# Kernel optimization log

Measured on AMD Instinct MI355X. Metric: run time of the kernel, lower is better.

## Reference

```python
import jax, jax.numpy as jnp
import numpy as np


def setup_inputs() -> dict:
    key = jax.random.key(0)
    k1, k2, k3 = jax.random.split(key, 3)
    B, S_enc, S_dec, D = 8, 4096, 4096, 128
    b = jax.random.normal(k1, (B, S_enc, D), dtype=jnp.float32)
    h = jax.random.normal(k2, (B, S_dec, D), dtype=jnp.float32)
    W_b = jax.random.normal(k3, (D, D), dtype=jnp.float32) * (1.0 / np.sqrt(D))
    return {"b": b, "h": h, "W_b": W_b}


def reference(b, h, W_b):
    # tmp1 = h @ W_b : [B, S_dec, D]
    tmp1 = jnp.einsum('btd,de->bte', h, W_b)
    # scores = tmp1 @ b^T : [B, S_dec, S_enc]
    scores = jnp.einsum('bte,bse->bts', tmp1, b)
    attn = jax.nn.softmax(scores, axis=-1)
    # weighted sum over encoder positions (the original does this via a huge
    # tile/broadcast/multiply/reduce_sum; math is a batched matmul)
    cxt = jnp.einsum('bts,bsd->btd', attn, b)
    return cxt
```

## Files before the change

kernel.cpp:

```cpp
#include <hip/hip_runtime.h>

typedef _Float16 half2v __attribute__((ext_vector_type(2)));
typedef _Float16 half4 __attribute__((ext_vector_type(4)));
typedef _Float16 half8 __attribute__((ext_vector_type(8)));
typedef float floatx4 __attribute__((ext_vector_type(4)));

#define B_   8
#define SE   4096
#define SD   4096
#define D_   128
#define NT   64
#define LDB  136
#define LOG2E 1.44269504f

__device__ __forceinline__ void cp16_async(const _Float16* g, _Float16* l) {
    __builtin_amdgcn_global_load_lds((const __attribute__((address_space(1))) unsigned int*)g,
                                     (__attribute__((address_space(3))) unsigned int*)l, 16, 0, 0);
}

__device__ __forceinline__ float dot2acc(half2v a, half2v b, float c) {
#if __has_builtin(__builtin_amdgcn_fdot2)
    return __builtin_amdgcn_fdot2(a, b, c, false);
#else
    return c + (float)a[0] * (float)b[0] + (float)a[1] * (float)b[1];
#endif
}

__global__ __launch_bounds__(256) void wprep(const float* __restrict__ W,
                                             _Float16* __restrict__ Wt16,
                                             _Float16* __restrict__ Wtlo) {
    int i = blockIdx.x * 256 + threadIdx.x;
    int d = i >> 7, e = i & 127;
    float w = W[i];
    _Float16 hi = (_Float16)w;
    Wt16[e * 128 + d] = hi;
    Wtlo[e * 128 + d] = (_Float16)(w - (float)hi);
}

__global__ __launch_bounds__(256) void bprep(const float* __restrict__ b,
                                             _Float16* __restrict__ kc,
                                             _Float16* __restrict__ vT) {
    __shared__ _Float16 bs[64 * LDB];
    const int bb = blockIdx.y, s0 = blockIdx.x * 64;
    const int tid = threadIdx.x;

    const float* bg = b + ((size_t)bb * SE + s0) * D_;
    _Float16* kg = kc + ((size_t)bb * SE + s0) * D_;
    #pragma unroll
    for (int it = 0; it < 4; ++it) {
        int idx = tid + it * 256;
        int row = idx >> 4, seg = idx & 15;
        const float* src = bg + row * D_ + seg * 8;
        float4 a = *(const float4*)src;
        float4 c = *(const float4*)(src + 4);
        half8 hv;
        hv[0] = (_Float16)a.x; hv[1] = (_Float16)a.y; hv[2] = (_Float16)a.z; hv[3] = (_Float16)a.w;
        hv[4] = (_Float16)c.x; hv[5] = (_Float16)c.y; hv[6] = (_Float16)c.z; hv[7] = (_Float16)c.w;
        *(half8*)(kg + row * D_ + seg * 8) = hv;
        *(half8*)(bs + row * LDB + seg * 8) = hv;
    }
    __syncthreads();

    const int sg = tid & 7, dg = tid >> 3;
    half4 rowv[8];
    #pragma unroll
    for (int j = 0; j < 8; ++j)
        rowv[j] = *(const half4*)(bs + (sg * 8 + j) * LDB + dg * 4);
    #pragma unroll
    for (int dd = 0; dd < 4; ++dd) {
        half8 o;
        #pragma unroll
        for (int j = 0; j < 8; ++j) o[j] = rowv[j][dd];
        *(half8*)(vT + ((size_t)bb * D_ + dg * 4 + dd) * SE + s0 + sg * 8) = o;
    }
}

__global__ __launch_bounds__(256, 2) void flash(const float* __restrict__ h,
                                                const _Float16* __restrict__ Wt16,
                                                const _Float16* __restrict__ Wtlo,
                                                const _Float16* __restrict__ kc,
                                                const _Float16* __restrict__ vT,
                                                float* __restrict__ out) {
    __shared__ _Float16 KV[2][16384];

    const int bb   = blockIdx.y;
    const int q0   = blockIdx.x * 64;
    const int tid  = threadIdx.x;
    const int wave = tid >> 6;
    const int wq   = wave >> 1;
    const int ws   = wave & 1;
    const int lane = tid & 63;
    const int l15  = lane & 15;
    const int quad = lane >> 4;

    const _Float16* kbase = kc + (size_t)bb * SE * D_;
    const _Float16* vbase = vT + (size_t)bb * D_ * SE;

    int koff[4], voff[4];
    #pragma unroll
    for (int it = 0; it < 4; ++it) {
        int i = it * 256 + wave * 64 + lane;
        int kr = i >> 4, kpp = i & 15;
        int km = kr & 15;
        int srow = (kr & 32) + ((km >> 2) << 3) + (((kr >> 4) & 1) << 2) + (km & 3);
        koff[it] = srow * D_ + ((kpp ^ km) * 8);
        int vr = i >> 3, vpp = i & 7;
        voff[it] = vr * SE + ((vpp ^ (vr & 7)) * 8);
    }

    const _Float16* kA0[4]; const _Float16* kA1[4];
    const _Float16 *vB0, *vB1;
    #pragma unroll
    for (int ks = 0; ks < 4; ++ks) {
        int o = l15 * 128 + (((ks * 4 + quad) ^ l15) * 8) + ws * 4096;
        kA0[ks] = &KV[0][o]; kA1[ks] = &KV[1][o];
    }
    {
        int o = 8192 + l15 * 64 + (((ws * 4 + quad) ^ (l15 & 7)) * 8);
        vB0 = &KV[0][o]; vB1 = &KV[1][o];
    }

    {
        _Float16* buf0 = &KV[0][0];
        #pragma unroll
        for (int it = 0; it < 4; ++it) {
            cp16_async(kbase + koff[it], buf0 + (it * 256 + wave * 64) * 8);
            cp16_async(vbase + voff[it], buf0 + 8192 + (it * 256 + wave * 64) * 8);
        }
    }

    _Float16* hs = &KV[1][0];
    {
        const float* hg = h + ((size_t)bb * SD + q0) * D_;
        #pragma unroll
        for (int it = 0; it < 4; ++it) {
            int idx = tid + it * 256;
            int row = idx >> 4, seg = idx & 15;
            const float* src = hg + row * D_ + seg * 8;
            float4 a = *(const float4*)src;
            float4 c = *(const float4*)(src + 4);
            half8 hv;
            hv[0] = (_Float16)a.x; hv[1] = (_Float16)a.y; hv[2] = (_Float16)a.z; hv[3] = (_Float16)a.w;
            hv[4] = (_Float16)c.x; hv[5] = (_Float16)c.y; hv[6] = (_Float16)c.z; hv[7] = (_Float16)c.w;
            *(half8*)(hs + row * LDB + seg * 8) = hv;
        }
    }
    __syncthreads();
    half8 qf0[4], qf1[4];
    {
        half8 af[4];
        #pragma unroll
        for (int ks = 0; ks < 4; ++ks)
            af[ks] = *(const half8*)(hs + (wave * 16 + l15) * LDB + ks * 32 + quad * 8);
        floatx4 acc[8];
        #pragma unroll
        for (int nt = 0; nt < 8; ++nt) acc[nt] = (floatx4){0.f, 0.f, 0.f, 0.f};
        #pragma unroll
        for (int ks = 0; ks < 4; ++ks) {
            #pragma unroll
            for (int nt = 0; nt < 8; ++nt) {
                half8 bh = *(const half8*)(Wt16 + (size_t)(nt * 16 + l15) * 128 + ks * 32 + quad * 8);
                half8 bl = *(const half8*)(Wtlo + (size_t)(nt * 16 + l15) * 128 + ks * 32 + quad * 8);
                acc[nt] = __builtin_amdgcn_mfma_f32_16x16x32_f16(af[ks], bh, acc[nt], 0, 0, 0);
                acc[nt] = __builtin_amdgcn_mfma_f32_16x16x32_f16(af[ks], bl, acc[nt], 0, 0, 0);
            }
        }
        __syncthreads();
        #pragma unroll
        for (int nt = 0; nt < 8; ++nt)
            #pragma unroll
            for (int r = 0; r < 4; ++r)
                hs[(wave * 16 + quad * 4 + r) * LDB + nt * 16 + l15] =
                    (_Float16)(acc[nt][r] * LOG2E);
        __syncthreads();
        #pragma unroll
        for (int ks = 0; ks < 4; ++ks) {
            qf0[ks] = *(const half8*)(hs + (wq * 32 + l15) * LDB + ks * 32 + quad * 8);
            qf1[ks] = *(const half8*)(hs + (wq * 32 + 16 + l15) * LDB + ks * 32 + quad * 8);
        }
    }

    floatx4 acc_o0[8], acc_o1[8];
    #pragma unroll
    for (int dt = 0; dt < 8; ++dt) {
        acc_o0[dt] = (floatx4){0.f, 0.f, 0.f, 0.f};
        acc_o1[dt] = (floatx4){0.f, 0.f, 0.f, 0.f};
    }
    float nm0 = 0.f, nm1 = 0.f;
    float lp0 = 0.f, lp1 = 0.f;
    const half2v one2 = { (_Float16)1.f, (_Float16)1.f };

#define RESCALE(MV, NM, LP, ACCS, ACCO)                                               \
    { float mr = fmaxf((MV), __shfl_xor((MV), 16, 64));                               \
      mr = fmaxf(mr, __shfl_xor(mr, 32, 64));                                         \
      float delta = fmaxf(mr, 0.f);                                                   \
      float alpha = exp2f(-delta);                                                    \
      LP *= alpha;                                                                    \
      float ab[4];                                                                    \
      _Pragma("unroll")                                                               \
      for (int r = 0; r < 4; ++r) ab[r] = __shfl(alpha, quad * 4 + r, 64);            \
      _Pragma("unroll")                                                               \
      for (int dt = 0; dt < 8; ++dt)                                                  \
        _Pragma("unroll")                                                             \
        for (int r = 0; r < 4; ++r) ACCO[dt][r] *= ab[r];                             \
      _Pragma("unroll")                                                               \
      for (int stl = 0; stl < 2; ++stl)                                               \
        _Pragma("unroll")                                                             \
        for (int r = 0; r < 4; ++r) ACCS[stl][r] -= delta;                            \
      NM -= delta; }

#define SOFTPACK(ACCS, LP, PA)                                                        \
    { float p0 = exp2f(ACCS[0][0]), p1 = exp2f(ACCS[0][1]);                           \
      float p2 = exp2f(ACCS[0][2]), p3 = exp2f(ACCS[0][3]);                           \
      float p4 = exp2f(ACCS[1][0]), p5 = exp2f(ACCS[1][1]);                           \
      float p6 = exp2f(ACCS[1][2]), p7 = exp2f(ACCS[1][3]);                           \
      half2v c0 = __builtin_bit_cast(half2v, __builtin_amdgcn_cvt_pkrtz(p0, p1));     \
      half2v c1 = __builtin_bit_cast(half2v, __builtin_amdgcn_cvt_pkrtz(p2, p3));     \
      half2v c2 = __builtin_bit_cast(half2v, __builtin_amdgcn_cvt_pkrtz(p4, p5));     \
      half2v c3 = __builtin_bit_cast(half2v, __builtin_amdgcn_cvt_pkrtz(p6, p7));     \
      LP = dot2acc(c0, one2, LP);                                                     \
      LP = dot2acc(c1, one2, LP);                                                     \
      LP = dot2acc(c2, one2, LP);                                                     \
      LP = dot2acc(c3, one2, LP);                                                     \
      PA[0] = c0[0]; PA[1] = c0[1]; PA[2] = c1[0]; PA[3] = c1[1];                     \
      PA[4] = c2[0]; PA[5] = c2[1]; PA[6] = c3[0]; PA[7] = c3[1]; }

#define STEP(T, KA, VBP, NBUF)                                                        \
  {                                                                                   \
    __syncthreads();                  \
    if ((T) + 1 < SE / NT) {                                                          \
      const _Float16* kt = kbase + (size_t)((T) + 1) * (NT * D_);                     \
      const _Float16* vt = vbase + (size_t)((T) + 1) * NT;                            \
      _Float16* bufn = (NBUF);                                                        \
      _Pragma("unroll")                                                               \
      for (int it = 0; it < 4; ++it) {                                                \
        cp16_async(kt + koff[it], bufn + (it * 256 + wave * 64) * 8);                 \
        cp16_async(vt + voff[it], bufn + 8192 + (it * 256 + wave * 64) * 8);          \
      }                                                                               \
    }                                                                                 \
    floatx4 accs0[2], accs1[2];                                                       \
    accs0[0] = (floatx4){nm0, nm0, nm0, nm0}; accs0[1] = accs0[0];                    \
    accs1[0] = (floatx4){nm1, nm1, nm1, nm1}; accs1[1] = accs1[0];                    \
    _Pragma("unroll")                                                                 \
    for (int ks = 0; ks < 4; ++ks) {                                                  \
      half8 af0 = *(const half8*)(KA[ks]);                                            \
      half8 af1 = *(const half8*)(KA[ks] + 2048);                                     \
      accs0[0] = __builtin_amdgcn_mfma_f32_16x16x32_f16(af0, qf0[ks], accs0[0], 0, 0, 0); \
      accs0[1] = __builtin_amdgcn_mfma_f32_16x16x32_f16(af1, qf0[ks], accs0[1], 0, 0, 0); \
      accs1[0] = __builtin_amdgcn_mfma_f32_16x16x32_f16(af0, qf1[ks], accs1[0], 0, 0, 0); \
      accs1[1] = __builtin_amdgcn_mfma_f32_16x16x32_f16(af1, qf1[ks], accs1[1], 0, 0, 0); \
    }                                                                                 \
    float mv0 = fmaxf(fmaxf(fmaxf(accs0[0][0], accs0[0][1]), fmaxf(accs0[0][2], accs0[0][3])), \
                      fmaxf(fmaxf(accs0[1][0], accs0[1][1]), fmaxf(accs0[1][2], accs0[1][3]))); \
    float mv1 = fmaxf(fmaxf(fmaxf(accs1[0][0], accs1[0][1]), fmaxf(accs1[0][2], accs1[0][3])), \
                      fmaxf(fmaxf(accs1[1][0], accs1[1][1]), fmaxf(accs1[1][2], accs1[1][3]))); \
    if (__ballot((mv0 > 11.5f) || (mv1 > 11.5f)) != 0ull) {                           \
      RESCALE(mv0, nm0, lp0, accs0, acc_o0);                                          \
      RESCALE(mv1, nm1, lp1, accs1, acc_o1);                                          \
    }                                                                                 \
    half8 pA0, pA1;                                                                   \
    SOFTPACK(accs0, lp0, pA0);                                                        \
    SOFTPACK(accs1, lp1, pA1);                                                        \
    _Pragma("unroll")                                                                 \
    for (int dt = 0; dt < 8; ++dt) {                                                  \
      half8 vf = *(const half8*)((VBP) + dt * 1024);                                  \
      acc_o0[dt] = __builtin_amdgcn_mfma_f32_16x16x32_f16(pA0, vf, acc_o0[dt], 0, 0, 0); \
      acc_o1[dt] = __builtin_amdgcn_mfma_f32_16x16x32_f16(pA1, vf, acc_o1[dt], 0, 0, 0); \
    }                                                                                 \
  }

    for (int t = 0; t < SE / NT; t += 2) {
        STEP(t,     kA0, vB0, &KV[1][0]);
        STEP(t + 1, kA1, vB1, &KV[0][0]);
    }
#undef STEP

    const float m_q0 = -nm0, m_q1 = -nm1;
    float lo0, lo1;
    {
        float l = lp0;
        l += __shfl_xor(l, 16, 64);
        l += __shfl_xor(l, 32, 64);
        lo0 = l;
        l = lp1;
        l += __shfl_xor(l, 16, 64);
        l += __shfl_xor(l, 32, 64);
        lo1 = l;
    }

    __syncthreads();
    float* Ob = (float*)&KV[0][0];
    float* ml = (float*)&KV[1][0];

    if (ws == 1) {
        #pragma unroll
        for (int dt = 0; dt < 8; ++dt) {
            *(floatx4*)(Ob + (((wq * 2 + 0) * 8 + dt) * 64 + lane) * 4) = acc_o0[dt];
            *(floatx4*)(Ob + (((wq * 2 + 1) * 8 + dt) * 64 + lane) * 4) = acc_o1[dt];
        }
        if (quad == 0) {
            *(float2*)(ml + (wq * 32 + l15) * 2)      = make_float2(m_q0, lo0);
            *(float2*)(ml + (wq * 32 + 16 + l15) * 2) = make_float2(m_q1, lo1);
        }
    }
    __syncthreads();
    if (ws == 0) {
#define MERGE(ACC, MQ, LO, QQ)                                                        \
      { float m0r[4], l0r[4], m1r[4], l1r[4];                                         \
        _Pragma("unroll")                                                             \
        for (int r = 0; r < 4; ++r) {                                                 \
            m0r[r] = __shfl((MQ), quad * 4 + r, 64);                                  \
            l0r[r] = __shfl((LO), quad * 4 + r, 64);                                  \
            float2 p = *(float2*)(ml + (wq * 32 + (QQ) * 16 + quad * 4 + r) * 2);     \
            m1r[r] = p.x; l1r[r] = p.y;                                               \
        }                                                                             \
        float a0[4], a1[4], inv[4];                                                   \
        _Pragma("unroll")                                                             \
        for (int r = 0; r < 4; ++r) {                                                 \
            float mm = fmaxf(m0r[r], m1r[r]);                                         \
            a0[r] = exp2f(m0r[r] - mm);                                               \
            a1[r] = exp2f(m1r[r] - mm);                                               \
            inv[r] = 1.f / (l0r[r] * a0[r] + l1r[r] * a1[r]);                         \
        }                                                                             \
        float* orow = out + ((size_t)bb * SD + q0 + wq * 32 + (QQ) * 16 + quad * 4) * D_; \
        _Pragma("unroll")                                                             \
        for (int dt = 0; dt < 8; ++dt) {                                              \
            floatx4 o1 = *(floatx4*)(Ob + (((wq * 2 + (QQ)) * 8 + dt) * 64 + lane) * 4); \
            _Pragma("unroll")                                                         \
            for (int r = 0; r < 4; ++r)                                               \
                orow[(size_t)r * D_ + dt * 16 + l15] =                                \
                    (ACC[dt][r] * a0[r] + o1[r] * a1[r]) * inv[r];                    \
        } }
        MERGE(acc_o0, m_q0, lo0, 0);
        MERGE(acc_o1, m_q1, lo1, 1);
#undef MERGE
    }
#undef RESCALE
#undef SOFTPACK
}

extern "C" void kernel_launch(void* const* d_in, const int* in_sizes, int n_in,
                              void* d_out, int out_size, void* d_ws, size_t ws_size,
                              hipStream_t stream) {
    const float* b = (const float*)d_in[0];
    const float* h = (const float*)d_in[1];
    const float* W = (const float*)d_in[2];
    float* out = (float*)d_out;

    _Float16* Wt16 = (_Float16*)d_ws;
    _Float16* Wtlo = Wt16 + 128 * 128;
    _Float16* kc   = Wtlo + 128 * 128;
    _Float16* vT   = kc + (size_t)B_ * SE * D_;

    wprep<<<64, 256, 0, stream>>>(W, Wt16, Wtlo);
    bprep<<<dim3(SE / 64, B_), 256, 0, stream>>>(b, kc, vT);
    flash<<<dim3(SD / 64, B_), 256, 0, stream>>>(h, Wt16, Wtlo, kc, vT, out);
}
```

Measured before the change: 199.3 us.

## Split encoder keys across two grid slices, widen blocks, add merge kernel

Splits the key/value sequence into two halves along a new grid z dimension, so each block computes partial softmax-weighted outputs and writes unnormalized results plus max/sum stats to global scratch. A separate merge kernel then combines the two partials. Blocks grow to 512 threads covering 128 queries, and the W prep is folded into bprep to save a launch. The aim is more parallelism and occupancy per key pass, at the cost of extra global traffic for the partials and one more launch.

```diff
diff --git a/kernel.cpp b/kernel.cpp
--- a/kernel.cpp
+++ b/kernel.cpp
@@ -10,6 +10,8 @@
 #define SD   4096
 #define D_   128
 #define NT   64
+#define NZ   2
+#define TILES (SE / NZ / NT)
 #define LDB  136
 #define LOG2E 1.44269504f
 
@@ -26,23 +28,28 @@
 #endif
 }
 
-__global__ __launch_bounds__(256) void wprep(const float* __restrict__ W,
+__global__ __launch_bounds__(256) void bprep(const float* __restrict__ b,
+                                             const float* __restrict__ W,
+                                             _Float16* __restrict__ kc,
+                                             _Float16* __restrict__ vT,
                                              _Float16* __restrict__ Wt16,
                                              _Float16* __restrict__ Wtlo) {
-    int i = blockIdx.x * 256 + threadIdx.x;
-    int d = i >> 7, e = i & 127;
-    float w = W[i];
-    _Float16 hi = (_Float16)w;
-    Wt16[e * 128 + d] = hi;
-    Wtlo[e * 128 + d] = (_Float16)(w - (float)hi);
-}
-
-__global__ __launch_bounds__(256) void bprep(const float* __restrict__ b,
-                                             _Float16* __restrict__ kc,
-                                             _Float16* __restrict__ vT) {
     __shared__ _Float16 bs[64 * LDB];
     const int bb = blockIdx.y, s0 = blockIdx.x * 64;
     const int tid = threadIdx.x;
+
+    if (blockIdx.x == 0) {
+        int base = bb * 2048 + tid * 8;
+        #pragma unroll
+        for (int j = 0; j < 8; ++j) {
+            int i = base + j;
+            int d = i >> 7, e = i & 127;
+            float w = W[i];
+            _Float16 hi = (_Float16)w;
+            Wt16[e * 128 + d] = hi;
+            Wtlo[e * 128 + d] = (_Float16)(w - (float)hi);
+        }
+    }
 
     const float* bg = b + ((size_t)bb * SE + s0) * D_;
     _Float16* kg = kc + ((size_t)bb * SE + s0) * D_;
@@ -75,16 +82,20 @@
     }
 }
 
-__global__ __launch_bounds__(256, 2) void flash(const float* __restrict__ h,
+__global__ __launch_bounds__(512, 4) void flash(const float* __restrict__ h,
                                                 const _Float16* __restrict__ Wt16,
                                                 const _Float16* __restrict__ Wtlo,
                                                 const _Float16* __restrict__ kc,
                                                 const _Float16* __restrict__ vT,
-                                                float* __restrict__ out) {
+                                                float* __restrict__ out,
+                                                float* __restrict__ P1,
+                                                float2* __restrict__ mlA,
+                                                float2* __restrict__ mlB) {
     __shared__ _Float16 KV[2][16384];
 
     const int bb   = blockIdx.y;
-    const int q0   = blockIdx.x * 64;
+    const int q0   = blockIdx.x * 128;
+    const int z    = blockIdx.z;
     const int tid  = threadIdx.x;
     const int wave = tid >> 6;
     const int wq   = wave >> 1;
@@ -93,13 +104,13 @@
     const int l15  = lane & 15;
     const int quad = lane >> 4;
 
-    const _Float16* kbase = kc + (size_t)bb * SE * D_;
-    const _Float16* vbase = vT + (size_t)bb * D_ * SE;
-
-    int koff[4], voff[4];
-    #pragma unroll
-    for (int it = 0; it < 4; ++it) {
-        int i = it * 256 + wave * 64 + lane;
+    const _Float16* kbase = kc + (size_t)bb * SE * D_ + (size_t)z * (SE / NZ) * D_;
+    const _Float16* vbase = vT + (size_t)bb * D_ * SE + (size_t)z * (SE / NZ);
+
+    int koff[2], voff[2];
+    #pragma unroll
+    for (int it = 0; it < 2; ++it) {
+        int i = it * 512 + wave * 64 + lane;
         int kr = i >> 4, kpp = i & 15;
         int km = kr & 15;
         int srow = (kr & 32) + ((km >> 2) << 3) + (((kr >> 4) & 1) << 2) + (km & 3);
@@ -123,18 +134,19 @@
     {
         _Float16* buf0 = &KV[0][0];
         #pragma unroll
-        for (int it = 0; it < 4; ++it) {
-            cp16_async(kbase + koff[it], buf0 + (it * 256 + wave * 64) * 8);
-            cp16_async(vbase + voff[it], buf0 + 8192 + (it * 256 + wave * 64) * 8);
+        for (int it = 0; it < 2; ++it) {
+            cp16_async(kbase + koff[it], buf0 + (it * 512 + wave * 64) * 8);
+            cp16_async(vbase + voff[it], buf0 + 8192 + (it * 512 + wave * 64) * 8);
         }
     }
 
     _Float16* hs = &KV[1][0];
+    const float* hg = h + ((size_t)bb * SD + q0) * D_;
+    half8 af[4];
     {
-        const float* hg = h + ((size_t)bb * SD + q0) * D_;
-        #pragma unroll
-        for (int it = 0; it < 4; ++it) {
-            int idx = tid + it * 256;
+        #pragma unroll
+        for (int it = 0; it < 2; ++it) {
+            int idx = tid + it * 512;
             int row = idx >> 4, seg = idx & 15;
             const float* src = hg + row * D_ + seg * 8;
             float4 a = *(const float4*)src;
@@ -144,14 +156,35 @@
             hv[4] = (_Float16)c.x; hv[5] = (_Float16)c.y; hv[6] = (_Float16)c.z; hv[7] = (_Float16)c.w;
             *(half8*)(hs + row * LDB + seg * 8) = hv;
         }
-    }
-    __syncthreads();
+        __syncthreads();
+        if (wave < 4) {
+            #pragma unroll
+            for (int ks = 0; ks < 4; ++ks)
+                af[ks] = *(const half8*)(hs + (wave * 16 + l15) * LDB + ks * 32 + quad * 8);
+        }
+        __syncthreads();
+        #pragma unroll
+        for (int it = 0; it < 2; ++it) {
+            int idx = tid + it * 512;
+            int row = idx >> 4, seg = idx & 15;
+            const float* src = hg + (row + 64) * D_ + seg * 8;
+            float4 a = *(const float4*)src;
+            float4 c = *(const float4*)(src + 4);
+            half8 hv;
+            hv[0] = (_Float16)a.x; hv[1] = (_Float16)a.y; hv[2] = (_Float16)a.z; hv[3] = (_Float16)a.w;
+            hv[4] = (_Float16)c.x; hv[5] = (_Float16)c.y; hv[6] = (_Float16)c.z; hv[7] = (_Float16)c.w;
+            *(half8*)(hs + row * LDB + seg * 8) = hv;
+        }
+        __syncthreads();
+        if (wave >= 4) {
+            #pragma unroll
+            for (int ks = 0; ks < 4; ++ks)
+                af[ks] = *(const half8*)(hs + ((wave - 4) * 16 + l15) * LDB + ks * 32 + quad * 8);
+        }
+        __syncthreads();
+    }
     half8 qf0[4], qf1[4];
     {
-        half8 af[4];
-        #pragma unroll
-        for (int ks = 0; ks < 4; ++ks)
-            af[ks] = *(const half8*)(hs + (wave * 16 + l15) * LDB + ks * 32 + quad * 8);
         floatx4 acc[8];
         #pragma unroll
         for (int nt = 0; nt < 8; ++nt) acc[nt] = (floatx4){0.f, 0.f, 0.f, 0.f};
@@ -159,24 +192,45 @@
         for (int ks = 0; ks < 4; ++ks) {
             #pragma unroll
             for (int nt = 0; nt < 8; ++nt) {
-                half8 bh = *(const half8*)(Wt16 + (size_t)(nt * 16 + l15) * 128 + ks * 32 + quad * 8);
-                half8 bl = *(const half8*)(Wtlo + (size_t)(nt * 16 + l15) * 128 + ks * 32 + quad * 8);
+                size_t wo = (size_t)(nt * 16 + l15) * 128 + ks * 32 + quad * 8;
+                half8 bh = *(const half8*)(Wt16 + wo);
+                half8 bl = *(const half8*)(Wtlo + wo);
                 acc[nt] = __builtin_amdgcn_mfma_f32_16x16x32_f16(af[ks], bh, acc[nt], 0, 0, 0);
                 acc[nt] = __builtin_amdgcn_mfma_f32_16x16x32_f16(af[ks], bl, acc[nt], 0, 0, 0);
             }
         }
-        __syncthreads();
-        #pragma unroll
-        for (int nt = 0; nt < 8; ++nt)
-            #pragma unroll
-            for (int r = 0; r < 4; ++r)
-                hs[(wave * 16 + quad * 4 + r) * LDB + nt * 16 + l15] =
-                    (_Float16)(acc[nt][r] * LOG2E);
-        __syncthreads();
-        #pragma unroll
-        for (int ks = 0; ks < 4; ++ks) {
-            qf0[ks] = *(const half8*)(hs + (wq * 32 + l15) * LDB + ks * 32 + quad * 8);
-            qf1[ks] = *(const half8*)(hs + (wq * 32 + 16 + l15) * LDB + ks * 32 + quad * 8);
+        if (wave < 4) {
+            #pragma unroll
+            for (int nt = 0; nt < 8; ++nt)
+                #pragma unroll
+                for (int r = 0; r < 4; ++r)
+                    hs[(wave * 16 + quad * 4 + r) * LDB + nt * 16 + l15] =
+                        (_Float16)(acc[nt][r] * LOG2E);
+        }
+        __syncthreads();
+        if (wq < 2) {
+            #pragma unroll
+            for (int ks = 0; ks < 4; ++ks) {
+                qf0[ks] = *(const half8*)(hs + (wq * 32 + l15) * LDB + ks * 32 + quad * 8);
+                qf1[ks] = *(const half8*)(hs + (wq * 32 + 16 + l15) * LDB + ks * 32 + quad * 8);
+            }
+        }
+        __syncthreads();
+        if (wave >= 4) {
+            #pragma unroll
+            for (int nt = 0; nt < 8; ++nt)
+                #pragma unroll
+                for (int r = 0; r < 4; ++r)
+                    hs[((wave - 4) * 16 + quad * 4 + r) * LDB + nt * 16 + l15] =
+                        (_Float16)(acc[nt][r] * LOG2E);
+        }
+        __syncthreads();
+        if (wq >= 2) {
+            #pragma unroll
+            for (int ks = 0; ks < 4; ++ks) {
+                qf0[ks] = *(const half8*)(hs + ((wq - 2) * 32 + l15) * LDB + ks * 32 + quad * 8);
+                qf1[ks] = *(const half8*)(hs + ((wq - 2) * 32 + 16 + l15) * LDB + ks * 32 + quad * 8);
+            }
         }
     }
 
@@ -228,14 +282,14 @@
 #define STEP(T, KA, VBP, NBUF)                                                        \
   {                                                                                   \
     __syncthreads();                  \
-    if ((T) + 1 < SE / NT) {                                                          \
+    if ((T) + 1 < TILES) {                                                            \
       const _Float16* kt = kbase + (size_t)((T) + 1) * (NT * D_);                     \
       const _Float16* vt = vbase + (size_t)((T) + 1) * NT;                            \
       _Float16* bufn = (NBUF);                                                        \
       _Pragma("unroll")                                                               \
-      for (int it = 0; it < 4; ++it) {                                                \
-        cp16_async(kt + koff[it], bufn + (it * 256 + wave * 64) * 8);                 \
-        cp16_async(vt + voff[it], bufn + 8192 + (it * 256 + wave * 64) * 8);          \
+      for (int it = 0; it < 2; ++it) {                                                \
+        cp16_async(kt + koff[it], bufn + (it * 512 + wave * 64) * 8);                 \
+        cp16_async(vt + voff[it], bufn + 8192 + (it * 512 + wave * 64) * 8);          \
       }                                                                               \
     }                                                                                 \
     floatx4 accs0[2], accs1[2];                                                       \
@@ -269,7 +323,7 @@
     }                                                                                 \
   }
 
-    for (int t = 0; t < SE / NT; t += 2) {
+    for (int t = 0; t < TILES; t += 2) {
         STEP(t,     kA0, vB0, &KV[1][0]);
         STEP(t + 1, kA1, vB1, &KV[0][0]);
     }
@@ -289,54 +343,87 @@
     }
 
     __syncthreads();
-    float* Ob = (float*)&KV[0][0];
-    float* ml = (float*)&KV[1][0];
+    float*  Ob  = (float*)&KV[0][0];
+    float2* mlb = (float2*)&KV[1][0];
+
+    float* dstO = (z == 0) ? out : P1;
+    float2* dstml = (z == 0) ? mlA : mlB;
 
     if (ws == 1) {
         #pragma unroll
-        for (int dt = 0; dt < 8; ++dt) {
-            *(floatx4*)(Ob + (((wq * 2 + 0) * 8 + dt) * 64 + lane) * 4) = acc_o0[dt];
-            *(floatx4*)(Ob + (((wq * 2 + 1) * 8 + dt) * 64 + lane) * 4) = acc_o1[dt];
-        }
+        for (int dt = 0; dt < 8; ++dt)
+            *(floatx4*)(Ob + ((wq * 8 + dt) * 64 + lane) * 4) = acc_o0[dt];
         if (quad == 0) {
-            *(float2*)(ml + (wq * 32 + l15) * 2)      = make_float2(m_q0, lo0);
-            *(float2*)(ml + (wq * 32 + 16 + l15) * 2) = make_float2(m_q1, lo1);
+            mlb[wq * 32 + l15]      = make_float2(m_q0, lo0);
+            mlb[wq * 32 + 16 + l15] = make_float2(m_q1, lo1);
         }
     }
     __syncthreads();
-    if (ws == 0) {
-#define MERGE(ACC, MQ, LO, QQ)                                                        \
-      { float m0r[4], l0r[4], m1r[4], l1r[4];                                         \
-        _Pragma("unroll")                                                             \
-        for (int r = 0; r < 4; ++r) {                                                 \
-            m0r[r] = __shfl((MQ), quad * 4 + r, 64);                                  \
-            l0r[r] = __shfl((LO), quad * 4 + r, 64);                                  \
-            float2 p = *(float2*)(ml + (wq * 32 + (QQ) * 16 + quad * 4 + r) * 2);     \
-            m1r[r] = p.x; l1r[r] = p.y;                                               \
-        }                                                                             \
-        float a0[4], a1[4], inv[4];                                                   \
-        _Pragma("unroll")                                                             \
-        for (int r = 0; r < 4; ++r) {                                                 \
-            float mm = fmaxf(m0r[r], m1r[r]);                                         \
-            a0[r] = exp2f(m0r[r] - mm);                                               \
-            a1[r] = exp2f(m1r[r] - mm);                                               \
-            inv[r] = 1.f / (l0r[r] * a0[r] + l1r[r] * a1[r]);                         \
-        }                                                                             \
-        float* orow = out + ((size_t)bb * SD + q0 + wq * 32 + (QQ) * 16 + quad * 4) * D_; \
-        _Pragma("unroll")                                                             \
-        for (int dt = 0; dt < 8; ++dt) {                                              \
-            floatx4 o1 = *(floatx4*)(Ob + (((wq * 2 + (QQ)) * 8 + dt) * 64 + lane) * 4); \
-            _Pragma("unroll")                                                         \
-            for (int r = 0; r < 4; ++r)                                               \
-                orow[(size_t)r * D_ + dt * 16 + l15] =                                \
-                    (ACC[dt][r] * a0[r] + o1[r] * a1[r]) * inv[r];                    \
-        } }
-        MERGE(acc_o0, m_q0, lo0, 0);
-        MERGE(acc_o1, m_q1, lo1, 1);
-#undef MERGE
-    }
+
+#define COMBINE(ACC, MQ, LO, QQ)                                                      \
+    { float m0r[4], l0r[4], m1r[4], l1r[4];                                           \
+      _Pragma("unroll")                                                               \
+      for (int r = 0; r < 4; ++r) {                                                   \
+          m0r[r] = __shfl((MQ), quad * 4 + r, 64);                                    \
+          l0r[r] = __shfl((LO), quad * 4 + r, 64);                                    \
+          float2 p = mlb[wq * 32 + (QQ) * 16 + quad * 4 + r];                         \
+          m1r[r] = p.x; l1r[r] = p.y;                                                 \
+      }                                                                               \
+      float a0[4], a1[4], mm[4], lc[4];                                               \
+      _Pragma("unroll")                                                               \
+      for (int r = 0; r < 4; ++r) {                                                   \
+          mm[r] = fmaxf(m0r[r], m1r[r]);                                              \
+          a0[r] = exp2f(m0r[r] - mm[r]);                                              \
+          a1[r] = exp2f(m1r[r] - mm[r]);                                              \
+          lc[r] = l0r[r] * a0[r] + l1r[r] * a1[r];                                    \
+      }                                                                               \
+      size_t qrow = (size_t)bb * SD + q0 + wq * 32 + (QQ) * 16 + quad * 4;            \
+      float* orow = dstO + qrow * D_;                                                 \
+      _Pragma("unroll")                                                               \
+      for (int dt = 0; dt < 8; ++dt) {                                                \
+          floatx4 o1 = *(floatx4*)(Ob + ((wq * 8 + dt) * 64 + lane) * 4);             \
+          _Pragma("unroll")                                                           \
+          for (int r = 0; r < 4; ++r)                                                 \
+              orow[(size_t)r * D_ + dt * 16 + l15] =                                  \
+                  ACC[dt][r] * a0[r] + o1[r] * a1[r];                                 \
+      }                                                                               \
+      if (l15 == 0) {                                                                 \
+          _Pragma("unroll")                                                           \
+          for (int r = 0; r < 4; ++r) dstml[qrow + r] = make_float2(mm[r], lc[r]);    \
+      } }
+
+    if (ws == 0) COMBINE(acc_o0, m_q0, lo0, 0);
+    __syncthreads();
+    if (ws == 1) {
+        #pragma unroll
+        for (int dt = 0; dt < 8; ++dt)
+            *(floatx4*)(Ob + ((wq * 8 + dt) * 64 + lane) * 4) = acc_o1[dt];
+    }
+    __syncthreads();
+    if (ws == 0) COMBINE(acc_o1, m_q1, lo1, 1);
+#undef COMBINE
 #undef RESCALE
 #undef SOFTPACK
+}
+
+__global__ __launch_bounds__(256) void merge(float* __restrict__ out,
+                                             const float* __restrict__ P1,
+                                             const float2* __restrict__ mlA,
+                                             const float2* __restrict__ mlB) {
+    int idx = blockIdx.x * 256 + threadIdx.x;
+    int row = idx >> 5;
+    float2 A = mlA[row], Bp = mlB[row];
+    float mm = fmaxf(A.x, Bp.x);
+    float a0 = exp2f(A.x - mm), a1 = exp2f(Bp.x - mm);
+    float inv = 1.f / (A.y * a0 + Bp.y * a1);
+    float4 o0 = ((const float4*)out)[idx];
+    float4 o1 = ((const float4*)P1)[idx];
+    float4 rlt;
+    rlt.x = (o0.x * a0 + o1.x * a1) * inv;
+    rlt.y = (o0.y * a0 + o1.y * a1) * inv;
+    rlt.z = (o0.z * a0 + o1.z * a1) * inv;
+    rlt.w = (o0.w * a0 + o1.w * a1) * inv;
+    ((float4*)out)[idx] = rlt;
 }
 
 extern "C" void kernel_launch(void* const* d_in, const int* in_sizes, int n_in,
@@ -351,8 +438,12 @@
     _Float16* Wtlo = Wt16 + 128 * 128;
     _Float16* kc   = Wtlo + 128 * 128;
     _Float16* vT   = kc + (size_t)B_ * SE * D_;
-
-    wprep<<<64, 256, 0, stream>>>(W, Wt16, Wtlo);
-    bprep<<<dim3(SE / 64, B_), 256, 0, stream>>>(b, kc, vT);
-    flash<<<dim3(SD / 64, B_), 256, 0, stream>>>(h, Wt16, Wtlo, kc, vT, out);
-}
+    float*    P1   = (float*)(vT + (size_t)B_ * D_ * SE);
+    float2*   mlA  = (float2*)(P1 + (size_t)B_ * SD * D_);
+    float2*   mlB  = mlA + (size_t)B_ * SD;
+
+    bprep<<<dim3(SE / 64, B_), 256, 0, stream>>>(b, W, kc, vT, Wt16, Wtlo);
+    flash<<<dim3(SD / 128, B_, NZ), 512, 0, stream>>>(h, Wt16, Wtlo, kc, vT,
+                                                      out, P1, mlA, mlB);
+    merge<<<(B_ * SD * D_ / 4) / 256, 256, 0, stream>>>(out, P1, mlA, mlB);
+}
```

New measurement: 294.1 us. 47.6% more time.

## Split flash KV tile across four waves per query group and fold W prep into bprep

Applied to the files above, without the earlier changes.

The flash kernel moves from 256 to 512 threads, so each query pair of 32 rows now has four waves splitting the 64-key tile, each owning 16 keys. The PV product switches to 16x16x16 MFMAs on half4 fragments. The final merge combines four partial softmax states through LDS in two staged passes. The W transpose/split kernel is folded into bprep's first column of blocks, removing one launch. This raises wave-level parallelism and latency hiding per block, at the cost of more LDS merge traffic and extra syncs, smaller MFMA shapes, and more register pressure under launch_bounds(512,4).

```diff
diff --git a/kernel.cpp b/kernel.cpp
--- a/kernel.cpp
+++ b/kernel.cpp
@@ -26,23 +26,28 @@
 #endif
 }
 
-__global__ __launch_bounds__(256) void wprep(const float* __restrict__ W,
+__global__ __launch_bounds__(256) void bprep(const float* __restrict__ b,
+                                             const float* __restrict__ W,
+                                             _Float16* __restrict__ kc,
+                                             _Float16* __restrict__ vT,
                                              _Float16* __restrict__ Wt16,
                                              _Float16* __restrict__ Wtlo) {
-    int i = blockIdx.x * 256 + threadIdx.x;
-    int d = i >> 7, e = i & 127;
-    float w = W[i];
-    _Float16 hi = (_Float16)w;
-    Wt16[e * 128 + d] = hi;
-    Wtlo[e * 128 + d] = (_Float16)(w - (float)hi);
-}
-
-__global__ __launch_bounds__(256) void bprep(const float* __restrict__ b,
-                                             _Float16* __restrict__ kc,
-                                             _Float16* __restrict__ vT) {
     __shared__ _Float16 bs[64 * LDB];
     const int bb = blockIdx.y, s0 = blockIdx.x * 64;
     const int tid = threadIdx.x;
+
+    if (blockIdx.x == 0) {
+        int base = bb * 2048 + tid * 8;
+        #pragma unroll
+        for (int j = 0; j < 8; ++j) {
+            int i = base + j;
+            int d = i >> 7, e = i & 127;
+            float w = W[i];
+            _Float16 hi = (_Float16)w;
+            Wt16[e * 128 + d] = hi;
+            Wtlo[e * 128 + d] = (_Float16)(w - (float)hi);
+        }
+    }
 
     const float* bg = b + ((size_t)bb * SE + s0) * D_;
     _Float16* kg = kc + ((size_t)bb * SE + s0) * D_;
@@ -75,7 +80,7 @@
     }
 }
 
-__global__ __launch_bounds__(256, 2) void flash(const float* __restrict__ h,
+__global__ __launch_bounds__(512, 4) void flash(const float* __restrict__ h,
                                                 const _Float16* __restrict__ Wt16,
                                                 const _Float16* __restrict__ Wtlo,
                                                 const _Float16* __restrict__ kc,
@@ -87,8 +92,8 @@
     const int q0   = blockIdx.x * 64;
     const int tid  = threadIdx.x;
     const int wave = tid >> 6;
-    const int wq   = wave >> 1;
-    const int ws   = wave & 1;
+    const int wq   = wave >> 2;
+    const int ws   = wave & 3;
     const int lane = tid & 63;
     const int l15  = lane & 15;
     const int quad = lane >> 4;
@@ -96,14 +101,12 @@
     const _Float16* kbase = kc + (size_t)bb * SE * D_;
     const _Float16* vbase = vT + (size_t)bb * D_ * SE;
 
-    int koff[4], voff[4];
-    #pragma unroll
-    for (int it = 0; it < 4; ++it) {
-        int i = it * 256 + wave * 64 + lane;
+    int koff[2], voff[2];
+    #pragma unroll
+    for (int it = 0; it < 2; ++it) {
+        int i = it * 512 + wave * 64 + lane;
         int kr = i >> 4, kpp = i & 15;
-        int km = kr & 15;
-        int srow = (kr & 32) + ((km >> 2) << 3) + (((kr >> 4) & 1) << 2) + (km & 3);
-        koff[it] = srow * D_ + ((kpp ^ km) * 8);
+        koff[it] = kr * D_ + ((kpp ^ (kr & 15)) * 8);
         int vr = i >> 3, vpp = i & 7;
         voff[it] = vr * SE + ((vpp ^ (vr & 7)) * 8);
     }
@@ -112,20 +115,20 @@
     const _Float16 *vB0, *vB1;
     #pragma unroll
     for (int ks = 0; ks < 4; ++ks) {
-        int o = l15 * 128 + (((ks * 4 + quad) ^ l15) * 8) + ws * 4096;
+        int o = ws * 2048 + l15 * 128 + (((ks * 4 + quad) ^ l15) * 8);
         kA0[ks] = &KV[0][o]; kA1[ks] = &KV[1][o];
     }
     {
-        int o = 8192 + l15 * 64 + (((ws * 4 + quad) ^ (l15 & 7)) * 8);
+        int o = 8192 + l15 * 64 + (((ws * 2 + (quad >> 1)) ^ (l15 & 7)) * 8) + (quad & 1) * 4;
         vB0 = &KV[0][o]; vB1 = &KV[1][o];
     }
 
     {
         _Float16* buf0 = &KV[0][0];
         #pragma unroll
-        for (int it = 0; it < 4; ++it) {
-            cp16_async(kbase + koff[it], buf0 + (it * 256 + wave * 64) * 8);
-            cp16_async(vbase + voff[it], buf0 + 8192 + (it * 256 + wave * 64) * 8);
+        for (int it = 0; it < 2; ++it) {
+            cp16_async(kbase + koff[it], buf0 + (it * 512 + wave * 64) * 8);
+            cp16_async(vbase + voff[it], buf0 + 8192 + (it * 512 + wave * 64) * 8);
         }
     }
 
@@ -133,8 +136,8 @@
     {
         const float* hg = h + ((size_t)bb * SD + q0) * D_;
         #pragma unroll
-        for (int it = 0; it < 4; ++it) {
-            int idx = tid + it * 256;
+        for (int it = 0; it < 2; ++it) {
+            int idx = tid + it * 512;
             int row = idx >> 4, seg = idx & 15;
             const float* src = hg + row * D_ + seg * 8;
             float4 a = *(const float4*)src;
@@ -148,29 +151,31 @@
     __syncthreads();
     half8 qf0[4], qf1[4];
     {
+        const int pwq = wave >> 1, pws = wave & 1;
         half8 af[4];
         #pragma unroll
         for (int ks = 0; ks < 4; ++ks)
-            af[ks] = *(const half8*)(hs + (wave * 16 + l15) * LDB + ks * 32 + quad * 8);
-        floatx4 acc[8];
-        #pragma unroll
-        for (int nt = 0; nt < 8; ++nt) acc[nt] = (floatx4){0.f, 0.f, 0.f, 0.f};
+            af[ks] = *(const half8*)(hs + (pwq * 16 + l15) * LDB + ks * 32 + quad * 8);
+        floatx4 acc[4];
+        #pragma unroll
+        for (int nt = 0; nt < 4; ++nt) acc[nt] = (floatx4){0.f, 0.f, 0.f, 0.f};
         #pragma unroll
         for (int ks = 0; ks < 4; ++ks) {
             #pragma unroll
-            for (int nt = 0; nt < 8; ++nt) {
-                half8 bh = *(const half8*)(Wt16 + (size_t)(nt * 16 + l15) * 128 + ks * 32 + quad * 8);
-                half8 bl = *(const half8*)(Wtlo + (size_t)(nt * 16 + l15) * 128 + ks * 32 + quad * 8);
+            for (int nt = 0; nt < 4; ++nt) {
+                size_t wo = (size_t)(pws * 64 + nt * 16 + l15) * 128 + ks * 32 + quad * 8;
+                half8 bh = *(const half8*)(Wt16 + wo);
+                half8 bl = *(const half8*)(Wtlo + wo);
                 acc[nt] = __builtin_amdgcn_mfma_f32_16x16x32_f16(af[ks], bh, acc[nt], 0, 0, 0);
                 acc[nt] = __builtin_amdgcn_mfma_f32_16x16x32_f16(af[ks], bl, acc[nt], 0, 0, 0);
             }
         }
         __syncthreads();
         #pragma unroll
-        for (int nt = 0; nt < 8; ++nt)
+        for (int nt = 0; nt < 4; ++nt)
             #pragma unroll
             for (int r = 0; r < 4; ++r)
-                hs[(wave * 16 + quad * 4 + r) * LDB + nt * 16 + l15] =
+                hs[(pwq * 16 + quad * 4 + r) * LDB + pws * 64 + nt * 16 + l15] =
                     (_Float16)(acc[nt][r] * LOG2E);
         __syncthreads();
         #pragma unroll
@@ -204,26 +209,17 @@
         _Pragma("unroll")                                                             \
         for (int r = 0; r < 4; ++r) ACCO[dt][r] *= ab[r];                             \
       _Pragma("unroll")                                                               \
-      for (int stl = 0; stl < 2; ++stl)                                               \
-        _Pragma("unroll")                                                             \
-        for (int r = 0; r < 4; ++r) ACCS[stl][r] -= delta;                            \
+      for (int r = 0; r < 4; ++r) ACCS[r] -= delta;                                   \
       NM -= delta; }
 
 #define SOFTPACK(ACCS, LP, PA)                                                        \
-    { float p0 = exp2f(ACCS[0][0]), p1 = exp2f(ACCS[0][1]);                           \
-      float p2 = exp2f(ACCS[0][2]), p3 = exp2f(ACCS[0][3]);                           \
-      float p4 = exp2f(ACCS[1][0]), p5 = exp2f(ACCS[1][1]);                           \
-      float p6 = exp2f(ACCS[1][2]), p7 = exp2f(ACCS[1][3]);                           \
+    { float p0 = exp2f(ACCS[0]), p1 = exp2f(ACCS[1]);                                 \
+      float p2 = exp2f(ACCS[2]), p3 = exp2f(ACCS[3]);                                 \
       half2v c0 = __builtin_bit_cast(half2v, __builtin_amdgcn_cvt_pkrtz(p0, p1));     \
       half2v c1 = __builtin_bit_cast(half2v, __builtin_amdgcn_cvt_pkrtz(p2, p3));     \
-      half2v c2 = __builtin_bit_cast(half2v, __builtin_amdgcn_cvt_pkrtz(p4, p5));     \
-      half2v c3 = __builtin_bit_cast(half2v, __builtin_amdgcn_cvt_pkrtz(p6, p7));     \
       LP = dot2acc(c0, one2, LP);                                                     \
       LP = dot2acc(c1, one2, LP);                                                     \
-      LP = dot2acc(c2, one2, LP);                                                     \
-      LP = dot2acc(c3, one2, LP);                                                     \
-      PA[0] = c0[0]; PA[1] = c0[1]; PA[2] = c1[0]; PA[3] = c1[1];                     \
-      PA[4] = c2[0]; PA[5] = c2[1]; PA[6] = c3[0]; PA[7] = c3[1]; }
+      PA[0] = c0[0]; PA[1] = c0[1]; PA[2] = c1[0]; PA[3] = c1[1]; }
 
 #define STEP(T, KA, VBP, NBUF)                                                        \
   {                                                                                   \
@@ -233,39 +229,36 @@
       const _Float16* vt = vbase + (size_t)((T) + 1) * NT;                            \
       _Float16* bufn = (NBUF);                                                        \
       _Pragma("unroll")                                                               \
-      for (int it = 0; it < 4; ++it) {                                                \
-        cp16_async(kt + koff[it], bufn + (it * 256 + wave * 64) * 8);                 \
-        cp16_async(vt + voff[it], bufn + 8192 + (it * 256 + wave * 64) * 8);          \
+      for (int it = 0; it < 2; ++it) {                                                \
+        cp16_async(kt + koff[it], bufn + (it * 512 + wave * 64) * 8);                 \
+        cp16_async(vt + voff[it], bufn + 8192 + (it * 512 + wave * 64) * 8);          \
       }                                                                               \
     }                                                                                 \
-    floatx4 accs0[2], accs1[2];                                                       \
-    accs0[0] = (floatx4){nm0, nm0, nm0, nm0}; accs0[1] = accs0[0];                    \
-    accs1[0] = (floatx4){nm1, nm1, nm1, nm1}; accs1[1] = accs1[0];                    \
+                              \
+    floatx4 accs0 = (floatx4){nm0, nm0, nm0, nm0};                                    \
+    floatx4 accs1 = (floatx4){nm1, nm1, nm1, nm1};                                    \
     _Pragma("unroll")                                                                 \
     for (int ks = 0; ks < 4; ++ks) {                                                  \
-      half8 af0 = *(const half8*)(KA[ks]);                                            \
-      half8 af1 = *(const half8*)(KA[ks] + 2048);                                     \
-      accs0[0] = __builtin_amdgcn_mfma_f32_16x16x32_f16(af0, qf0[ks], accs0[0], 0, 0, 0); \
-      accs0[1] = __builtin_amdgcn_mfma_f32_16x16x32_f16(af1, qf0[ks], accs0[1], 0, 0, 0); \
-      accs1[0] = __builtin_amdgcn_mfma_f32_16x16x32_f16(af0, qf1[ks], accs1[0], 0, 0, 0); \
-      accs1[1] = __builtin_amdgcn_mfma_f32_16x16x32_f16(af1, qf1[ks], accs1[1], 0, 0, 0); \
+      half8 af = *(const half8*)(KA[ks]);                                             \
+      accs0 = __builtin_amdgcn_mfma_f32_16x16x32_f16(af, qf0[ks], accs0, 0, 0, 0);    \
+      accs1 = __builtin_amdgcn_mfma_f32_16x16x32_f16(af, qf1[ks], accs1, 0, 0, 0);    \
     }                                                                                 \
-    float mv0 = fmaxf(fmaxf(fmaxf(accs0[0][0], accs0[0][1]), fmaxf(accs0[0][2], accs0[0][3])), \
-                      fmaxf(fmaxf(accs0[1][0], accs0[1][1]), fmaxf(accs0[1][2], accs0[1][3]))); \
-    float mv1 = fmaxf(fmaxf(fmaxf(accs1[0][0], accs1[0][1]), fmaxf(accs1[0][2], accs1[0][3])), \
-                      fmaxf(fmaxf(accs1[1][0], accs1[1][1]), fmaxf(accs1[1][2], accs1[1][3]))); \
+    float mv0 = fmaxf(fmaxf(accs0[0], accs0[1]), fmaxf(accs0[2], accs0[3]));          \
+    float mv1 = fmaxf(fmaxf(accs1[0], accs1[1]), fmaxf(accs1[2], accs1[3]));          \
     if (__ballot((mv0 > 11.5f) || (mv1 > 11.5f)) != 0ull) {                           \
       RESCALE(mv0, nm0, lp0, accs0, acc_o0);                                          \
       RESCALE(mv1, nm1, lp1, accs1, acc_o1);                                          \
     }                                                                                 \
-    half8 pA0, pA1;                                                                   \
-    SOFTPACK(accs0, lp0, pA0);                                                        \
-    SOFTPACK(accs1, lp1, pA1);                                                        \
+                     \
+    half4 pf0, pf1;                                                                   \
+    SOFTPACK(accs0, lp0, pf0);                                                        \
+    SOFTPACK(accs1, lp1, pf1);                                                        \
+           \
     _Pragma("unroll")                                                                 \
     for (int dt = 0; dt < 8; ++dt) {                                                  \
-      half8 vf = *(const half8*)((VBP) + dt * 1024);                                  \
-      acc_o0[dt] = __builtin_amdgcn_mfma_f32_16x16x32_f16(pA0, vf, acc_o0[dt], 0, 0, 0); \
-      acc_o1[dt] = __builtin_amdgcn_mfma_f32_16x16x32_f16(pA1, vf, acc_o1[dt], 0, 0, 0); \
+      half4 vf = *(const half4*)((VBP) + dt * 1024);                                  \
+      acc_o0[dt] = __builtin_amdgcn_mfma_f32_16x16x16f16(pf0, vf, acc_o0[dt], 0, 0, 0); \
+      acc_o1[dt] = __builtin_amdgcn_mfma_f32_16x16x16f16(pf1, vf, acc_o1[dt], 0, 0, 0); \
     }                                                                                 \
   }
 
@@ -289,52 +282,60 @@
     }
 
     __syncthreads();
-    float* Ob = (float*)&KV[0][0];
-    float* ml = (float*)&KV[1][0];
-
-    if (ws == 1) {
-        #pragma unroll
-        for (int dt = 0; dt < 8; ++dt) {
-            *(floatx4*)(Ob + (((wq * 2 + 0) * 8 + dt) * 64 + lane) * 4) = acc_o0[dt];
-            *(floatx4*)(Ob + (((wq * 2 + 1) * 8 + dt) * 64 + lane) * 4) = acc_o1[dt];
-        }
-        if (quad == 0) {
-            *(float2*)(ml + (wq * 32 + l15) * 2)      = make_float2(m_q0, lo0);
-            *(float2*)(ml + (wq * 32 + 16 + l15) * 2) = make_float2(m_q1, lo1);
-        }
-    }
-    __syncthreads();
-    if (ws == 0) {
-#define MERGE(ACC, MQ, LO, QQ)                                                        \
-      { float m0r[4], l0r[4], m1r[4], l1r[4];                                         \
+    float*  Ob  = (float*)&KV[0][0];
+    float2* mlb = (float2*)((float*)&KV[0][0] + 12288);
+
+#define STAGE_COMBINE(ACC, MQ, LO, QQ)                                                \
+    { if (ws != 0) {                                                                  \
+        _Pragma("unroll")                                                             \
+        for (int dt = 0; dt < 8; ++dt)                                                \
+            *(floatx4*)(Ob + (((wq * 3 + ws - 1) * 8 + dt) * 64 + lane) * 4) = ACC[dt]; \
+        if (quad == 0)                                                                \
+            mlb[(wq * 4 + ws) * 16 + l15] = make_float2((MQ), (LO));                  \
+      }                                                                               \
+      __syncthreads();                                                                \
+      if (ws == 0) {                                                                  \
+        float mr_[4][4], lr_[4][4];                                                   \
         _Pragma("unroll")                                                             \
         for (int r = 0; r < 4; ++r) {                                                 \
-            m0r[r] = __shfl((MQ), quad * 4 + r, 64);                                  \
-            l0r[r] = __shfl((LO), quad * 4 + r, 64);                                  \
-            float2 p = *(float2*)(ml + (wq * 32 + (QQ) * 16 + quad * 4 + r) * 2);     \
-            m1r[r] = p.x; l1r[r] = p.y;                                               \
+            mr_[0][r] = __shfl((MQ), quad * 4 + r, 64);                               \
+            lr_[0][r] = __shfl((LO), quad * 4 + r, 64);                               \
+            _Pragma("unroll")                                                         \
+            for (int w = 1; w < 4; ++w) {                                             \
+                float2 p = mlb[(wq * 4 + w) * 16 + quad * 4 + r];                     \
+                mr_[w][r] = p.x; lr_[w][r] = p.y;                                     \
+            }                                                                         \
         }                                                                             \
-        float a0[4], a1[4], inv[4];                                                   \
+        float aw[4][4], inv[4];                                                       \
         _Pragma("unroll")                                                             \
         for (int r = 0; r < 4; ++r) {                                                 \
-            float mm = fmaxf(m0r[r], m1r[r]);                                         \
-            a0[r] = exp2f(m0r[r] - mm);                                               \
-            a1[r] = exp2f(m1r[r] - mm);                                               \
-            inv[r] = 1.f / (l0r[r] * a0[r] + l1r[r] * a1[r]);                         \
+            float mm = fmaxf(fmaxf(mr_[0][r], mr_[1][r]), fmaxf(mr_[2][r], mr_[3][r])); \
+            float lc = 0.f;                                                           \
+            _Pragma("unroll")                                                         \
+            for (int w = 0; w < 4; ++w) {                                             \
+                aw[w][r] = exp2f(mr_[w][r] - mm);                                     \
+                lc += lr_[w][r] * aw[w][r];                                           \
+            }                                                                         \
+            inv[r] = 1.f / lc;                                                        \
         }                                                                             \
         float* orow = out + ((size_t)bb * SD + q0 + wq * 32 + (QQ) * 16 + quad * 4) * D_; \
         _Pragma("unroll")                                                             \
         for (int dt = 0; dt < 8; ++dt) {                                              \
-            floatx4 o1 = *(floatx4*)(Ob + (((wq * 2 + (QQ)) * 8 + dt) * 64 + lane) * 4); \
+            floatx4 o1 = *(floatx4*)(Ob + (((wq * 3 + 0) * 8 + dt) * 64 + lane) * 4); \
+            floatx4 o2 = *(floatx4*)(Ob + (((wq * 3 + 1) * 8 + dt) * 64 + lane) * 4); \
+            floatx4 o3 = *(floatx4*)(Ob + (((wq * 3 + 2) * 8 + dt) * 64 + lane) * 4); \
             _Pragma("unroll")                                                         \
             for (int r = 0; r < 4; ++r)                                               \
                 orow[(size_t)r * D_ + dt * 16 + l15] =                                \
-                    (ACC[dt][r] * a0[r] + o1[r] * a1[r]) * inv[r];                    \
-        } }
-        MERGE(acc_o0, m_q0, lo0, 0);
-        MERGE(acc_o1, m_q1, lo1, 1);
-#undef MERGE
-    }
+                    (ACC[dt][r] * aw[0][r] + o1[r] * aw[1][r] +                       \
+                     o2[r] * aw[2][r] + o3[r] * aw[3][r]) * inv[r];                   \
+        }                                                                             \
+      }                                                                               \
+      __syncthreads(); }
+
+    STAGE_COMBINE(acc_o0, m_q0, lo0, 0);
+    STAGE_COMBINE(acc_o1, m_q1, lo1, 1);
+#undef STAGE_COMBINE
 #undef RESCALE
 #undef SOFTPACK
 }
@@ -352,7 +353,6 @@
     _Float16* kc   = Wtlo + 128 * 128;
     _Float16* vT   = kc + (size_t)B_ * SE * D_;
 
-    wprep<<<64, 256, 0, stream>>>(W, Wt16, Wtlo);
-    bprep<<<dim3(SE / 64, B_), 256, 0, stream>>>(b, kc, vT);
-    flash<<<dim3(SD / 64, B_), 256, 0, stream>>>(h, Wt16, Wtlo, kc, vT, out);
-}
+    bprep<<<dim3(SE / 64, B_), 256, 0, stream>>>(b, W, kc, vT, Wt16, Wtlo);
+    flash<<<dim3(SD / 64, B_), 512, 0, stream>>>(h, Wt16, Wtlo, kc, vT, out);
+}
```

Result: slower. 322.8 us (+61.9%).
